# Optimization experiments

Measured on AMD Instinct MI355X. Metric: run time of the kernel, lower is better.

Reference implementation:

```python
import jax, jax.numpy as jnp
import numpy as np

BN_EPS = 1e-5
RENORM_EPS = 1e-9


def setup_inputs() -> dict:
    key = jax.random.key(0)
    ks = jax.random.split(key, 8)
    B, C, N = 4, 256, 4096
    D = C // 4
    return {
        "x": jax.random.normal(ks[0], (B, C, N), jnp.float32),
        "y": jax.random.normal(ks[1], (B, C, N), jnp.float32),
        "w_qkx": jax.random.normal(ks[2], (D, C), jnp.float32) / np.sqrt(C),
        "w_vx": jax.random.normal(ks[3], (C, C), jnp.float32) / np.sqrt(C),
        "w_tx": jax.random.normal(ks[4], (C, C), jnp.float32) / np.sqrt(C),
        "w_qky": jax.random.normal(ks[5], (D, C), jnp.float32) / np.sqrt(C),
        "w_vy": jax.random.normal(ks[6], (C, C), jnp.float32) / np.sqrt(C),
        "w_ty": jax.random.normal(ks[7], (C, C), jnp.float32) / np.sqrt(C),
        "gamma": jnp.ones((C,), jnp.float32),
        "beta": jnp.zeros((C,), jnp.float32),
    }


def _conv1x1(w, x):
    # w: (O, C), x: (B, C, N) -> (B, O, N)
    return jnp.einsum("oc,bcn->bon", w, x)


def _batchnorm1d(x, gamma, beta):
    # training-mode BN over (B, N) per channel, biased variance (torch default)
    mean = x.mean(axis=(0, 2), keepdims=True)
    var = ((x - mean) ** 2).mean(axis=(0, 2), keepdims=True)
    xhat = (x - mean) * jax.lax.rsqrt(var + BN_EPS)
    return gamma[None, :, None] * xhat + beta[None, :, None]


def _branch(src, tgt, w_qk, w_v, w_t, gamma, beta):
    # cross-attention: queries from tgt, keys/values from src; output length = len(tgt)
    q = _conv1x1(w_qk, tgt)          # (B, D, M)
    k = _conv1x1(w_qk, src)          # (B, D, N)
    v = _conv1x1(w_v, src)           # (B, C, N)
    energy = jnp.einsum("bdm,bdn->bmn", q, k)      # (B, M, N)
    att = jax.nn.softmax(energy, axis=-1)
    att = att / (RENORM_EPS + att.sum(axis=2, keepdims=True))  # extra L1 renorm
    r = jnp.einsum("bcn,bmn->bcm", v, att)         # (B, C, M)
    return jax.nn.relu(_batchnorm1d(_conv1x1(w_t, r), gamma, beta))


def reference(x, y, w_qkx, w_vx, w_tx, w_qky, w_vy, w_ty, gamma, beta):
    r_x = _branch(x, y, w_qkx, w_vx, w_tx, gamma, beta)  # queries from y, kv from x
    r_y = _branch(y, x, w_qky, w_vy, w_ty, gamma, beta)  # queries from x, kv from y
    return (x + r_x, y + r_y)
```

## Files before the change

kernel.cpp:

```cpp
#include <hip/hip_runtime.h>

constexpr int Bc = 4;
constexpr int Cc = 256;
constexpr int Dc = 64;
constexpr int Nc = 4096;

typedef __attribute__((ext_vector_type(8))) _Float16 f16x8;
typedef __attribute__((ext_vector_type(4))) _Float16 f16x4;
typedef __attribute__((ext_vector_type(4))) float f32x4;

__device__ inline void gload_lds16(const _Float16* g, _Float16* lds) {
  __builtin_amdgcn_global_load_lds(
      (const __attribute__((address_space(1))) unsigned int*)g,
      (__attribute__((address_space(3))) unsigned int*)lds, 16, 0, 0);
}

__global__ __launch_bounds__(256) void wconv_kernel(
    const float* __restrict__ Wvx, const float* __restrict__ Wvy,
    const float* __restrict__ Wtx, const float* __restrict__ Wty,
    const float* __restrict__ Wqkx, const float* __restrict__ Wqky,
    _Float16* __restrict__ Wh)
{
  const int i = blockIdx.x * 256 + threadIdx.x;
  const int z = blockIdx.y;
  if (z < 4) {
    const float* w = (z == 0) ? Wvx : (z == 1) ? Wvy : (z == 2) ? Wtx : Wty;
    Wh[(size_t)z * Cc * Cc + i] = (_Float16)w[i];
  } else if (i < Dc * Cc) {
    const float* w = (z == 4) ? Wqkx : Wqky;
    Wh[(size_t)4 * Cc * Cc + (size_t)(z - 4) * Dc * Cc + i] = (_Float16)w[i];
  }
}

__global__ __launch_bounds__(256) void transpose_kernel(
    const float* __restrict__ X, const float* __restrict__ Y,
    _Float16* __restrict__ Xt)
{
  __shared__ float tile[64][65];
  const int t  = threadIdx.x;
  const int n0 = blockIdx.x * 64;
  const int c0 = blockIdx.y * 64;
  const int z  = blockIdx.z, br = z >> 2, b = z & 3;
  const float* In = (br ? Y : X) + (size_t)b * Cc * Nc;
#pragma unroll
  for (int p = 0; p < 4; ++p) {
    const int c = p * 16 + (t >> 4), n4 = (t & 15) * 4;
    float4 v = *(const float4*)&In[(size_t)(c0 + c) * Nc + n0 + n4];
    tile[c][n4 + 0] = v.x; tile[c][n4 + 1] = v.y;
    tile[c][n4 + 2] = v.z; tile[c][n4 + 3] = v.w;
  }
  __syncthreads();
  _Float16* Ob = Xt + ((size_t)(br * Bc + b) * Nc + n0) * Cc + c0;
#pragma unroll
  for (int p = 0; p < 4; ++p) {
    const int n = p * 16 + (t >> 4), c4 = (t & 15) * 4;
    f16x4 w;
#pragma unroll
    for (int j = 0; j < 4; ++j) w[j] = (_Float16)tile[c4 + j][n];
    *(f16x4*)&Ob[(size_t)n * Cc + c4] = w;
  }
}

__global__ __launch_bounds__(256, 4) void conv_qk_mfma_kernel(
    const _Float16* __restrict__ Xt, const _Float16* __restrict__ Wh,
    _Float16* __restrict__ Qt, _Float16* __restrict__ Kt)
{
  const int t  = threadIdx.x;
  const int ws = t >> 6, l = t & 63, lr = l & 15, lg = l >> 4;
  const int n_w = blockIdx.x * 128 + ws * 32;
  const int qk = blockIdx.y;
  const int z  = blockIdx.z, br = z >> 2, b = z & 3;
  const size_t bb = (size_t)(br * Bc + b);
  const int insel = (qk ^ br ^ 1) & 1;
  _Float16* Out = qk ? Kt : Qt;

  const _Float16* wbase = Wh + (size_t)4 * Cc * Cc + (size_t)br * Dc * Cc
                          + (size_t)lr * Cc + lg * 8;
  const _Float16* xbase = Xt + ((size_t)(insel * Bc + b) * Nc + n_w + lr) * Cc + lg * 8;

  f32x4 acc[4][2] = {};
  for (int c0 = 0; c0 < Cc; c0 += 32) {
    f16x8 wf[4], xf[2];
#pragma unroll
    for (int dt = 0; dt < 4; ++dt)
      wf[dt] = *(const f16x8*)(wbase + (size_t)(dt * 16) * Cc + c0);
#pragma unroll
    for (int nt = 0; nt < 2; ++nt)
      xf[nt] = *(const f16x8*)(xbase + (size_t)(nt * 16) * Cc + c0);
#pragma unroll
    for (int dt = 0; dt < 4; ++dt)
#pragma unroll
      for (int nt = 0; nt < 2; ++nt)
        acc[dt][nt] = __builtin_amdgcn_mfma_f32_16x16x32_f16(wf[dt], xf[nt], acc[dt][nt], 0, 0, 0);
  }
#pragma unroll
  for (int dt = 0; dt < 4; ++dt)
#pragma unroll
    for (int nt = 0; nt < 2; ++nt) {
      const int n  = n_w + nt * 16 + lr;
      const int d0 = dt * 16 + lg * 4;
      const int off = qk ? (d0 ^ ((n & 7) << 3)) : d0;
      f16x4 o4;
#pragma unroll
      for (int r = 0; r < 4; ++r) o4[r] = (_Float16)acc[dt][nt][r];
      *(f16x4*)&Out[(bb * Nc + n) * 64 + off] = o4;
    }
}

__global__ __launch_bounds__(256, 4) void conv_v_mfma_kernel(
    const _Float16* __restrict__ Xt, const _Float16* __restrict__ Wh,
    _Float16* __restrict__ Vb)
{
  const int t  = threadIdx.x;
  const int ws = t >> 6, l = t & 63, lr = l & 15, lg = l >> 4;
  const int wm = ws >> 1, wo = ws & 1;
  const int n_w = blockIdx.x * 128 + wm * 64;
  const int o_w = blockIdx.y * 128 + wo * 64;
  const int z  = blockIdx.z, br = z >> 2, b = z & 3;
  const size_t bb = (size_t)(br * Bc + b);

  const _Float16* abase = Xt + (bb * Nc + n_w + lr) * Cc + lg * 8;
  const _Float16* bbase = Wh + ((size_t)br * Cc + o_w + lr) * Cc + lg * 8;
  f32x4 acc[4][4] = {};

  for (int c0 = 0; c0 < Cc; c0 += 32) {
    f16x8 af[4], bfr[4];
#pragma unroll
    for (int mt = 0; mt < 4; ++mt)
      af[mt] = *(const f16x8*)(abase + (size_t)(mt * 16) * Cc + c0);
#pragma unroll
    for (int ot = 0; ot < 4; ++ot)
      bfr[ot] = *(const f16x8*)(bbase + (size_t)(ot * 16) * Cc + c0);
#pragma unroll
    for (int ot = 0; ot < 4; ++ot)
#pragma unroll
      for (int mt = 0; mt < 4; ++mt)
        acc[ot][mt] = __builtin_amdgcn_mfma_f32_16x16x32_f16(af[mt], bfr[ot], acc[ot][mt], 0, 0, 0);
  }
#pragma unroll
  for (int ot = 0; ot < 4; ++ot)
#pragma unroll
    for (int mt = 0; mt < 4; ++mt) {
      const int cout = o_w + ot * 16 + lr;
      const int n = n_w + mt * 16 + lg * 4;
      f16x4 o4;
#pragma unroll
      for (int r = 0; r < 4; ++r) o4[r] = (_Float16)acc[ot][mt][r];
      *(f16x4*)&Vb[(bb * Cc + cout) * Nc + n] = o4;
    }
}

__global__ __launch_bounds__(256, 2) void attn_mfma_kernel(
    const _Float16* __restrict__ Qt,
    const _Float16* __restrict__ Kt,
    const _Float16* __restrict__ V,
    _Float16* __restrict__ Op,
    float* __restrict__ Ml,
    int nsp, int kn)
{
  __shared__ __align__(16) _Float16 k_lds[2][64 * 64];
  __shared__ __align__(16) _Float16 p_lds[2][64 * 64];
  __shared__ float s_fac[2][64];

  const int t  = threadIdx.x;
  const int ws = t >> 6;
  const int l  = t & 63;
  const int lr = l & 15;
  const int lg = l >> 4;

  const int nwg  = (Nc / 64) * nsp * 8;
  const int lin  = blockIdx.x + gridDim.x * (blockIdx.y + gridDim.y * blockIdx.z);
  const int work = (lin & 7) * (nwg >> 3) + (lin >> 3);
  const int m0   = (work & 63) * 64;
  const int spbb = work >> 6;
  const int sp   = spbb % nsp;
  const size_t bb = (size_t)(spbb / nsp);

  const _Float16* qp = Qt + (bb * Nc + m0 + ws * 16 + lr) * 64 + lg * 8;
  const f16x8 qf0 = *(const f16x8*)qp;
  const f16x8 qf1 = *(const f16x8*)(qp + 32);

  const _Float16* kgl   = Kt + (bb * Nc + (size_t)sp * kn) * 64;
  const _Float16* vbase = V + (bb * Cc + ws * 64 + lr) * Nc + sp * kn + lg * 8;

  float m_run = -1e30f, l_run = 0.f;
  f32x4 acc[4][4] = {};
  f16x8 vf[2][4][2];

  const int  mrow = ws * 16 + lr;
  const int  sw   = (mrow & 7) << 4;

  const _Float16* gq = kgl + ws * 512 + l * 8;

  {
#pragma unroll
    for (int r = 0; r < 2; ++r)
      gload_lds16(gq + r * 2048, &k_lds[0][ws * 512 + r * 2048]);
  }
  __syncthreads();

  const int nch = kn >> 6;
  for (int ch2 = 0; ch2 < nch; ch2 += 2) {
#pragma unroll
    for (int par = 0; par < 2; ++par) {
      const int ch = ch2 + par;
      if (ch + 1 < nch) {
        const _Float16* g = gq + (size_t)(ch + 1) * (64 * 64);
#pragma unroll
        for (int r = 0; r < 2; ++r)
          gload_lds16(g + r * 2048, &k_lds[par ^ 1][ws * 512 + r * 2048]);
      }
      {
        const _Float16* vp = vbase + ch * 64;
#pragma unroll
        for (int ct = 0; ct < 4; ++ct)
#pragma unroll
          for (int kk = 0; kk < 2; ++kk)
            vf[par][ct][kk] = *(const f16x8*)(vp + (size_t)ct * 16 * Nc + kk * 32);
      }
      if (ch > 0) {
        float scm[4];
#pragma unroll
        for (int mt = 0; mt < 4; ++mt) scm[mt] = s_fac[par ^ 1][mt * 16 + lr];
        const int needs = (scm[0] != 1.f) | (scm[1] != 1.f) |
                          (scm[2] != 1.f) | (scm[3] != 1.f);
        if (__any(needs)) {
#pragma unroll
          for (int ct = 0; ct < 4; ++ct)
#pragma unroll
            for (int mt = 0; mt < 4; ++mt) {
              acc[ct][mt][0] *= scm[mt]; acc[ct][mt][1] *= scm[mt];
              acc[ct][mt][2] *= scm[mt]; acc[ct][mt][3] *= scm[mt];
            }
        }
        f16x8 pf[4][2];
#pragma unroll
        for (int mt = 0; mt < 4; ++mt) {
          const int   rm  = mt * 16 + lr;
          const char* pr  = (const char*)&p_lds[par ^ 1][rm * 64];
          const int   swr = (rm & 7) << 4;
#pragma unroll
          for (int kk = 0; kk < 2; ++kk)
            pf[mt][kk] = *(const f16x8*)(pr + ((lg * 16 + kk * 64) ^ swr));
        }
        __builtin_amdgcn_s_setprio(1);
#pragma unroll
        for (int ct = 0; ct < 4; ++ct)
#pragma unroll
          for (int kk = 0; kk < 2; ++kk)
#pragma unroll
            for (int mt = 0; mt < 4; ++mt)
              acc[ct][mt] = __builtin_amdgcn_mfma_f32_16x16x32_f16(vf[par ^ 1][ct][kk], pf[mt][kk], acc[ct][mt], 0, 0, 0);
        __builtin_amdgcn_s_setprio(0);
      }

      f32x4 st[4] = {};
#pragma unroll
      for (int nt = 0; nt < 4; ++nt) {
        const int   krow = nt * 16 + lr;
        const char* krp  = (const char*)&k_lds[par][krow * 64];
        const int   swr  = (krow & 7) << 4;
        f16x8 kh0 = *(const f16x8*)(krp + ((lg * 16) ^ swr));
        f16x8 kh1 = *(const f16x8*)(krp + ((64 + lg * 16) ^ swr));
        st[nt] = __builtin_amdgcn_mfma_f32_16x16x32_f16(kh0, qf0, st[nt], 0, 0, 0);
        st[nt] = __builtin_amdgcn_mfma_f32_16x16x32_f16(kh1, qf1, st[nt], 0, 0, 0);
      }

      float mx = -1e30f;
#pragma unroll
      for (int nt = 0; nt < 4; ++nt)
#pragma unroll
        for (int rr = 0; rr < 4; ++rr) mx = fmaxf(mx, st[nt][rr]);
      mx = fmaxf(mx, __shfl_xor(mx, 16));
      mx = fmaxf(mx, __shfl_xor(mx, 32));
      const float mnew = fmaxf(m_run, mx);
      const float s = __expf(m_run - mnew);
      float p[4][4];
      float sum = 0.f;
#pragma unroll
      for (int nt = 0; nt < 4; ++nt)
#pragma unroll
        for (int rr = 0; rr < 4; ++rr) {
          p[nt][rr] = __expf(st[nt][rr] - mnew);
          sum += p[nt][rr];
        }
      sum += __shfl_xor(sum, 16);
      sum += __shfl_xor(sum, 32);
      l_run = l_run * s + sum;
      m_run = mnew;
      {
        char* prow = (char*)&p_lds[par][mrow * 64];
#pragma unroll
        for (int nt = 0; nt < 4; ++nt) {
          f16x4 pb;
          pb[0] = (_Float16)p[nt][0]; pb[1] = (_Float16)p[nt][1];
          pb[2] = (_Float16)p[nt][2]; pb[3] = (_Float16)p[nt][3];
          *(f16x4*)(prow + ((nt * 32 + lg * 8) ^ sw)) = pb;
        }
      }
      if (lg == 0) s_fac[par][ws * 16 + lr] = s;
      __syncthreads();
    }
  }

  {
    float scm[4];
#pragma unroll
    for (int mt = 0; mt < 4; ++mt) scm[mt] = s_fac[1][mt * 16 + lr];
    const int needs = (scm[0] != 1.f) | (scm[1] != 1.f) |
                      (scm[2] != 1.f) | (scm[3] != 1.f);
    if (__any(needs)) {
#pragma unroll
      for (int ct = 0; ct < 4; ++ct)
#pragma unroll
        for (int mt = 0; mt < 4; ++mt) {
          acc[ct][mt][0] *= scm[mt]; acc[ct][mt][1] *= scm[mt];
          acc[ct][mt][2] *= scm[mt]; acc[ct][mt][3] *= scm[mt];
        }
    }
    f16x8 pf[4][2];
#pragma unroll
    for (int mt = 0; mt < 4; ++mt) {
      const int   rm  = mt * 16 + lr;
      const char* pr  = (const char*)&p_lds[1][rm * 64];
      const int   swr = (rm & 7) << 4;
#pragma unroll
      for (int kk = 0; kk < 2; ++kk)
        pf[mt][kk] = *(const f16x8*)(pr + ((lg * 16 + kk * 64) ^ swr));
    }
#pragma unroll
    for (int ct = 0; ct < 4; ++ct)
#pragma unroll
      for (int kk = 0; kk < 2; ++kk)
#pragma unroll
        for (int mt = 0; mt < 4; ++mt)
          acc[ct][mt] = __builtin_amdgcn_mfma_f32_16x16x32_f16(vf[1][ct][kk], pf[mt][kk], acc[ct][mt], 0, 0, 0);
  }

  if (lg == 0) {
    size_t mi = ((bb * nsp + sp) * Nc + m0 + ws * 16 + lr) * 2;
    Ml[mi]     = m_run;
    Ml[mi + 1] = l_run;
  }
  _Float16* ob = Op + (bb * nsp + sp) * (size_t)Cc * Nc;
#pragma unroll
  for (int ct = 0; ct < 4; ++ct)
#pragma unroll
    for (int mt = 0; mt < 4; ++mt) {
      const int c0 = ws * 64 + ct * 16 + lg * 4;
      const int m  = m0 + mt * 16 + lr;
      f16x4 o4;
#pragma unroll
      for (int r = 0; r < 4; ++r) o4[r] = (_Float16)acc[ct][mt][r];
      *(f16x4*)&ob[(size_t)m * Cc + c0] = o4;
    }
}

__global__ __launch_bounds__(256) void combine_kernel(
    const _Float16* __restrict__ Op, const float* __restrict__ Ml,
    _Float16* __restrict__ Rt, int nsp)
{
  const int tid = blockIdx.x * 256 + threadIdx.x;
  const int c0 = (tid & 63) * 4;
  const int m  = (tid >> 6) & (Nc - 1);
  const int bb = tid >> 18;
  float val[4];
  if (nsp == 2) {
    const _Float16* o0 = Op + ((size_t)bb * 2 + 0) * Cc * Nc + (size_t)m * Cc + c0;
    const _Float16* o1 = Op + ((size_t)bb * 2 + 1) * Cc * Nc + (size_t)m * Cc + c0;
    const float* ml0 = Ml + (((size_t)bb * 2 + 0) * Nc + m) * 2;
    const float* ml1 = Ml + (((size_t)bb * 2 + 1) * Nc + m) * 2;
    float m1 = ml0[0], L1 = ml0[1], m2 = ml1[0], L2 = ml1[1];
    float M  = fmaxf(m1, m2);
    float w1 = __expf(m1 - M), w2 = __expf(m2 - M);
    float inv = 1.0f / (w1 * L1 + w2 * L2);
    f16x4 a = *(const f16x4*)o0;
    f16x4 d = *(const f16x4*)o1;
#pragma unroll
    for (int j = 0; j < 4; ++j) val[j] = (w1 * (float)a[j] + w2 * (float)d[j]) * inv;
  } else {
    const _Float16* o0 = Op + (size_t)bb * Cc * Nc + (size_t)m * Cc + c0;
    const float* ml0 = Ml + ((size_t)bb * Nc + m) * 2;
    float inv = 1.0f / ml0[1];
    f16x4 a = *(const f16x4*)o0;
#pragma unroll
    for (int j = 0; j < 4; ++j) val[j] = (float)a[j] * inv;
  }
  f16x4 r4;
#pragma unroll
  for (int j = 0; j < 4; ++j) r4[j] = (_Float16)val[j];
  *(f16x4*)&Rt[((size_t)bb * Nc + m) * Cc + c0] = r4;
}

__global__ __launch_bounds__(256, 4) void conv_t_mfma_kernel(
    const _Float16* __restrict__ Rt, const _Float16* __restrict__ Wh,
    float* __restrict__ T, float* __restrict__ part)
{
  __shared__ float red[2][2][4][16][2];
  const int t  = threadIdx.x;
  const int ws = t >> 6, l = t & 63, lr = l & 15, lg = l >> 4;
  const int wm = ws >> 1, wo = ws & 1;
  const int m_w = blockIdx.x * 128 + wm * 64;
  const int o_w = blockIdx.y * 128 + wo * 64;
  const int z  = blockIdx.z, br = z >> 2, b = z & 3;
  const size_t bb = (size_t)(br * Bc + b);

  const _Float16* abase = Rt + (bb * Nc + m_w + lr) * Cc + lg * 8;
  const _Float16* bbase = Wh + ((size_t)(2 + br) * Cc + o_w + lr) * Cc + lg * 8;
  f32x4 acc[4][4] = {};

  for (int c0 = 0; c0 < Cc; c0 += 32) {
    f16x8 af[4], bfr[4];
#pragma unroll
    for (int mt = 0; mt < 4; ++mt)
      af[mt] = *(const f16x8*)(abase + (size_t)(mt * 16) * Cc + c0);
#pragma unroll
    for (int ot = 0; ot < 4; ++ot)
      bfr[ot] = *(const f16x8*)(bbase + (size_t)(ot * 16) * Cc + c0);
#pragma unroll
    for (int ot = 0; ot < 4; ++ot)
#pragma unroll
      for (int mt = 0; mt < 4; ++mt)
        acc[ot][mt] = __builtin_amdgcn_mfma_f32_16x16x32_f16(af[mt], bfr[ot], acc[ot][mt], 0, 0, 0);
  }
  float* Tb = T + bb * Cc * Nc;
#pragma unroll
  for (int ot = 0; ot < 4; ++ot) {
    float s = 0.f, q = 0.f;
#pragma unroll
    for (int mt = 0; mt < 4; ++mt) {
      const int o = o_w + ot * 16 + lr;
      const int m = m_w + mt * 16 + lg * 4;
      *(f32x4*)&Tb[(size_t)o * Nc + m] = acc[ot][mt];
#pragma unroll
      for (int r = 0; r < 4; ++r) {
        float v = acc[ot][mt][r];
        s += v; q += v * v;
      }
    }
    s += __shfl_xor(s, 16); s += __shfl_xor(s, 32);
    q += __shfl_xor(q, 16); q += __shfl_xor(q, 32);
    if (lg == 0) { red[wm][wo][ot][lr][0] = s; red[wm][wo][ot][lr][1] = q; }
  }
  __syncthreads();
  {
    const int wo2 = t >> 7, ot2 = (t >> 5) & 3, lr2 = (t >> 1) & 15, kind = t & 1;
    float v = red[0][wo2][ot2][lr2][kind] + red[1][wo2][ot2][lr2][kind];
    const int c = blockIdx.y * 128 + wo2 * 64 + ot2 * 16 + lr2;
    const int slot = blockIdx.x * 4 + b;
    part[(((size_t)br * Cc + c) * 128 + slot) * 2 + kind] = v;
  }
}

__global__ __launch_bounds__(256) void bn_finalize_kernel(
    const float* __restrict__ part, float* __restrict__ stats)
{
  const int br = blockIdx.x, c = threadIdx.x;
  const float* p = part + ((size_t)br * Cc + c) * 128 * 2;
  float s = 0.f, q = 0.f;
#pragma unroll 4
  for (int i = 0; i < 128; ++i) { s += p[i * 2]; q += p[i * 2 + 1]; }
  const float inv_n = 1.0f / (float)(Bc * Nc);
  const float mean = s * inv_n;
  const float var  = q * inv_n - mean * mean;
  stats[(br * 2 + 0) * Cc + c] = mean;
  stats[(br * 2 + 1) * Cc + c] = rsqrtf(var + 1e-5f);
}

__global__ __launch_bounds__(256) void bn_out_kernel(
    float* __restrict__ TO,
    const float* __restrict__ X, const float* __restrict__ Y,
    const float* __restrict__ stats, const float* __restrict__ gamma,
    const float* __restrict__ beta)
{
  const int br = blockIdx.y;
  const int i = blockIdx.x * 256 + threadIdx.x;
  const size_t flat = ((size_t)i << 2);
  const int c = (int)((flat >> 12) & (Cc - 1));
  float mean = stats[(br * 2 + 0) * Cc + c], istd = stats[(br * 2 + 1) * Cc + c];
  float gm = gamma[c], bt = beta[c];
  float* Tb = TO + (size_t)br * Bc * Cc * Nc;
  const float* SRC = (br ? Y : X);
  float4 t4 = *(const float4*)&Tb[flat];
  float4 s4 = *(const float4*)&SRC[flat];
  float4 o4;
  o4.x = s4.x + fmaxf(0.f, gm * (t4.x - mean) * istd + bt);
  o4.y = s4.y + fmaxf(0.f, gm * (t4.y - mean) * istd + bt);
  o4.z = s4.z + fmaxf(0.f, gm * (t4.z - mean) * istd + bt);
  o4.w = s4.w + fmaxf(0.f, gm * (t4.w - mean) * istd + bt);
  *(float4*)&Tb[flat] = o4;
}

extern "C" void kernel_launch(void* const* d_in, const int* in_sizes, int n_in,
                              void* d_out, int out_size, void* d_ws, size_t ws_size,
                              hipStream_t stream) {
  const float* x     = (const float*)d_in[0];
  const float* y     = (const float*)d_in[1];
  const float* w_qkx = (const float*)d_in[2];
  const float* w_vx  = (const float*)d_in[3];
  const float* w_tx  = (const float*)d_in[4];
  const float* w_qky = (const float*)d_in[5];
  const float* w_vy  = (const float*)d_in[6];
  const float* w_ty  = (const float*)d_in[7];
  const float* gamma = (const float*)d_in[8];
  const float* beta  = (const float*)d_in[9];

  float* out = (float*)d_out;

  const int nsp = (ws_size >= 60ull * 1024 * 1024) ? 2 : 1;
  const int kn  = Nc / nsp;

  char* wsb = (char*)d_ws;
  _Float16* qt = (_Float16*)wsb;
  _Float16* kt = (_Float16*)(wsb + (4ull << 20));
  _Float16* vb = (_Float16*)(wsb + (8ull << 20));
  _Float16* xt = (_Float16*)(wsb + (24ull << 20));
  _Float16* op = (_Float16*)(wsb + (24ull << 20));
  size_t off = (24ull << 20) + (size_t)nsp * (16ull << 20);
  float* ml = (float*)(wsb + off);
  off += (size_t)nsp * (256ull << 10);
  _Float16* wh = (_Float16*)(wsb + off);
  off += (640ull << 10);
  float* part = (float*)(wsb + off);
  off += (512ull << 10);
  float* st = (float*)(wsb + off);
  _Float16* rt = (_Float16*)wsb;

  wconv_kernel<<<dim3(Cc * Cc / 256, 6), 256, 0, stream>>>(w_vx, w_vy, w_tx, w_ty, w_qkx, w_qky, wh);
  transpose_kernel<<<dim3(Nc / 64, Cc / 64, 8), 256, 0, stream>>>(x, y, xt);
  conv_qk_mfma_kernel<<<dim3(Nc / 128, 2, 8), 256, 0, stream>>>(xt, wh, qt, kt);
  conv_v_mfma_kernel<<<dim3(Nc / 128, Cc / 128, 8), 256, 0, stream>>>(xt, wh, vb);
  attn_mfma_kernel<<<dim3(Nc / 64, nsp, 8), 256, 0, stream>>>(qt, kt, vb, op, ml, nsp, kn);
  combine_kernel<<<(2 * Bc * Nc * (Cc / 4)) / 256, 256, 0, stream>>>(op, ml, rt, nsp);
  conv_t_mfma_kernel<<<dim3(Nc / 128, Cc / 128, 8), 256, 0, stream>>>(rt, wh, out, part);
  bn_finalize_kernel<<<2, 256, 0, stream>>>(part, st);
  bn_out_kernel<<<dim3((Bc * Cc * Nc / 4) / 256, 2), 256, 0, stream>>>(out, x, y, st, gamma, beta);
}
```

Before: 254.0 us.

## Use exp2 with prescaled queries, lazy softmax rescaling, fp16 conv_t intermediate

Queries are prescaled by log2(e) so the attention softmax can use the native exp2 instruction. The online-softmax max update is now lazy: the running max is only refreshed when a new score exceeds it by a threshold, and the per-row sum reductions are deferred to a single cross-lane reduction at the end. The conv_t output is stored as fp16 in workspace instead of fp32 in the output buffer, which halves the traffic between conv_t and the BN/residual kernel. The costs are lower precision in the BN input and possible exp overflow headroom issues if scores jump by up to the threshold.

```diff
diff --git a/kernel.cpp b/kernel.cpp
--- a/kernel.cpp
+++ b/kernel.cpp
@@ -8,6 +8,8 @@
 typedef __attribute__((ext_vector_type(8))) _Float16 f16x8;
 typedef __attribute__((ext_vector_type(4))) _Float16 f16x4;
 typedef __attribute__((ext_vector_type(4))) float f32x4;
+
+__device__ inline float exp2fast(float x) { return __builtin_amdgcn_exp2f(x); }
 
 __device__ inline void gload_lds16(const _Float16* g, _Float16* lds) {
   __builtin_amdgcn_global_load_lds(
@@ -73,6 +75,7 @@
   const size_t bb = (size_t)(br * Bc + b);
   const int insel = (qk ^ br ^ 1) & 1;
   _Float16* Out = qk ? Kt : Qt;
+  const float scale = qk ? 1.0f : 1.44269504088896f;
 
   const _Float16* wbase = Wh + (size_t)4 * Cc * Cc + (size_t)br * Dc * Cc
                           + (size_t)lr * Cc + lg * 8;
@@ -102,7 +105,7 @@
       const int off = qk ? (d0 ^ ((n & 7) << 3)) : d0;
       f16x4 o4;
 #pragma unroll
-      for (int r = 0; r < 4; ++r) o4[r] = (_Float16)acc[dt][nt][r];
+      for (int r = 0; r < 4; ++r) o4[r] = (_Float16)(acc[dt][nt][r] * scale);
       *(f16x4*)&Out[(bb * Nc + n) * 64 + off] = o4;
     }
 }
@@ -266,28 +269,29 @@
         st[nt] = __builtin_amdgcn_mfma_f32_16x16x32_f16(kh1, qf1, st[nt], 0, 0, 0);
       }
 
-      float mx = -1e30f;
+      float mx = st[0][0];
 #pragma unroll
       for (int nt = 0; nt < 4; ++nt)
 #pragma unroll
         for (int rr = 0; rr < 4; ++rr) mx = fmaxf(mx, st[nt][rr]);
-      mx = fmaxf(mx, __shfl_xor(mx, 16));
-      mx = fmaxf(mx, __shfl_xor(mx, 32));
-      const float mnew = fmaxf(m_run, mx);
-      const float s = __expf(m_run - mnew);
+      float s = 1.0f;
+      if (__any(mx > m_run + 12.0f)) {
+        mx = fmaxf(mx, __shfl_xor(mx, 16));
+        mx = fmaxf(mx, __shfl_xor(mx, 32));
+        const float mnew = fmaxf(m_run, mx);
+        s = exp2fast(m_run - mnew);
+        m_run = mnew;
+      }
+      float sum = 0.f;
       float p[4][4];
-      float sum = 0.f;
 #pragma unroll
       for (int nt = 0; nt < 4; ++nt)
 #pragma unroll
         for (int rr = 0; rr < 4; ++rr) {
-          p[nt][rr] = __expf(st[nt][rr] - mnew);
+          p[nt][rr] = exp2fast(st[nt][rr] - m_run);
           sum += p[nt][rr];
         }
-      sum += __shfl_xor(sum, 16);
-      sum += __shfl_xor(sum, 32);
       l_run = l_run * s + sum;
-      m_run = mnew;
       {
         char* prow = (char*)&p_lds[par][mrow * 64];
 #pragma unroll
@@ -336,6 +340,9 @@
         for (int mt = 0; mt < 4; ++mt)
           acc[ct][mt] = __builtin_amdgcn_mfma_f32_16x16x32_f16(vf[1][ct][kk], pf[mt][kk], acc[ct][mt], 0, 0, 0);
   }
+
+  l_run += __shfl_xor(l_run, 16);
+  l_run += __shfl_xor(l_run, 32);
 
   if (lg == 0) {
     size_t mi = ((bb * nsp + sp) * Nc + m0 + ws * 16 + lr) * 2;
@@ -372,7 +379,7 @@
     const float* ml1 = Ml + (((size_t)bb * 2 + 1) * Nc + m) * 2;
     float m1 = ml0[0], L1 = ml0[1], m2 = ml1[0], L2 = ml1[1];
     float M  = fmaxf(m1, m2);
-    float w1 = __expf(m1 - M), w2 = __expf(m2 - M);
+    float w1 = __builtin_amdgcn_exp2f(m1 - M), w2 = __builtin_amdgcn_exp2f(m2 - M);
     float inv = 1.0f / (w1 * L1 + w2 * L2);
     f16x4 a = *(const f16x4*)o0;
     f16x4 d = *(const f16x4*)o1;
@@ -394,7 +401,7 @@
 
 __global__ __launch_bounds__(256, 4) void conv_t_mfma_kernel(
     const _Float16* __restrict__ Rt, const _Float16* __restrict__ Wh,
-    float* __restrict__ T, float* __restrict__ part)
+    _Float16* __restrict__ Th, float* __restrict__ part)
 {
   __shared__ float red[2][2][4][16][2];
   const int t  = threadIdx.x;
@@ -423,7 +430,7 @@
       for (int mt = 0; mt < 4; ++mt)
         acc[ot][mt] = __builtin_amdgcn_mfma_f32_16x16x32_f16(af[mt], bfr[ot], acc[ot][mt], 0, 0, 0);
   }
-  float* Tb = T + bb * Cc * Nc;
+  _Float16* Tb = Th + bb * Cc * Nc;
 #pragma unroll
   for (int ot = 0; ot < 4; ++ot) {
     float s = 0.f, q = 0.f;
@@ -431,12 +438,14 @@
     for (int mt = 0; mt < 4; ++mt) {
       const int o = o_w + ot * 16 + lr;
       const int m = m_w + mt * 16 + lg * 4;
-      *(f32x4*)&Tb[(size_t)o * Nc + m] = acc[ot][mt];
+      f16x4 h4;
 #pragma unroll
       for (int r = 0; r < 4; ++r) {
         float v = acc[ot][mt][r];
+        h4[r] = (_Float16)v;
         s += v; q += v * v;
       }
+      *(f16x4*)&Tb[(size_t)o * Nc + m] = h4;
     }
     s += __shfl_xor(s, 16); s += __shfl_xor(s, 32);
     q += __shfl_xor(q, 16); q += __shfl_xor(q, 32);
@@ -468,7 +477,7 @@
 }
 
 __global__ __launch_bounds__(256) void bn_out_kernel(
-    float* __restrict__ TO,
+    const _Float16* __restrict__ Th, float* __restrict__ OUT,
     const float* __restrict__ X, const float* __restrict__ Y,
     const float* __restrict__ stats, const float* __restrict__ gamma,
     const float* __restrict__ beta)
@@ -479,16 +488,17 @@
   const int c = (int)((flat >> 12) & (Cc - 1));
   float mean = stats[(br * 2 + 0) * Cc + c], istd = stats[(br * 2 + 1) * Cc + c];
   float gm = gamma[c], bt = beta[c];
-  float* Tb = TO + (size_t)br * Bc * Cc * Nc;
+  const _Float16* Tb = Th + (size_t)br * Bc * Cc * Nc;
+  float* Ob = OUT + (size_t)br * Bc * Cc * Nc;
   const float* SRC = (br ? Y : X);
-  float4 t4 = *(const float4*)&Tb[flat];
+  f16x4 t4 = *(const f16x4*)&Tb[flat];
   float4 s4 = *(const float4*)&SRC[flat];
   float4 o4;
-  o4.x = s4.x + fmaxf(0.f, gm * (t4.x - mean) * istd + bt);
-  o4.y = s4.y + fmaxf(0.f, gm * (t4.y - mean) * istd + bt);
-  o4.z = s4.z + fmaxf(0.f, gm * (t4.z - mean) * istd + bt);
-  o4.w = s4.w + fmaxf(0.f, gm * (t4.w - mean) * istd + bt);
-  *(float4*)&Tb[flat] = o4;
+  o4.x = s4.x + fmaxf(0.f, gm * ((float)t4[0] - mean) * istd + bt);
+  o4.y = s4.y + fmaxf(0.f, gm * ((float)t4[1] - mean) * istd + bt);
+  o4.z = s4.z + fmaxf(0.f, gm * ((float)t4[2] - mean) * istd + bt);
+  o4.w = s4.w + fmaxf(0.f, gm * ((float)t4[3] - mean) * istd + bt);
+  *(float4*)&Ob[flat] = o4;
 }
 
 extern "C" void kernel_launch(void* const* d_in, const int* in_sizes, int n_in,
@@ -525,6 +535,7 @@
   off += (512ull << 10);
   float* st = (float*)(wsb + off);
   _Float16* rt = (_Float16*)wsb;
+  _Float16* th = (_Float16*)(wsb + (24ull << 20));
 
   wconv_kernel<<<dim3(Cc * Cc / 256, 6), 256, 0, stream>>>(w_vx, w_vy, w_tx, w_ty, w_qkx, w_qky, wh);
   transpose_kernel<<<dim3(Nc / 64, Cc / 64, 8), 256, 0, stream>>>(x, y, xt);
@@ -532,7 +543,7 @@
   conv_v_mfma_kernel<<<dim3(Nc / 128, Cc / 128, 8), 256, 0, stream>>>(xt, wh, vb);
   attn_mfma_kernel<<<dim3(Nc / 64, nsp, 8), 256, 0, stream>>>(qt, kt, vb, op, ml, nsp, kn);
   combine_kernel<<<(2 * Bc * Nc * (Cc / 4)) / 256, 256, 0, stream>>>(op, ml, rt, nsp);
-  conv_t_mfma_kernel<<<dim3(Nc / 128, Cc / 128, 8), 256, 0, stream>>>(rt, wh, out, part);
+  conv_t_mfma_kernel<<<dim3(Nc / 128, Cc / 128, 8), 256, 0, stream>>>(rt, wh, th, part);
   bn_finalize_kernel<<<2, 256, 0, stream>>>(part, st);
-  bn_out_kernel<<<dim3((Bc * Cc * Nc / 4) / 256, 2), 256, 0, stream>>>(out, x, y, st, gamma, beta);
-}
+  bn_out_kernel<<<dim3((Bc * Cc * Nc / 4) / 256, 2), 256, 0, stream>>>(th, out, x, y, st, gamma, beta);
+}
```

Result: no change. 249.8 us, median of 2 (-1.7%).
